# Optimization experiments

Hardware: AMD Instinct MI355X
Metric: run time of the kernel (lower is better)

The kernel has to match this reference:

```python
import jax, jax.numpy as jnp
import numpy as np

B, D, SLOTS, TOPK, CODE, ANCH = 8192, 64, 32, 3, 128, 32
BETA = 0.25  # vq_commitment_beta


def _clinear(zr, zi, Wr, Wi, br, bi):
    # ComplexLinear: real = Wr(zr)-Wi(zi), imag = Wi(zr)+Wr(zi); each nn.Linear carries its own bias
    return (zr @ Wr + br) - (zi @ Wi + bi), (zr @ Wi + bi) + (zi @ Wr + br)


def _layernorm(x, g, b, eps=1e-6):
    m = x.mean(-1, keepdims=True)
    v = ((x - m) ** 2).mean(-1, keepdims=True)  # biased var, as torch LayerNorm
    return (x - m) / jnp.sqrt(v + eps) * g + b


def setup_inputs() -> dict:
    key = jax.random.key(0)
    ks = jax.random.split(key, 16)
    f = jax.random.normal
    s = 0.05
    rng_init = 1.0 / np.sqrt(D)
    return dict(
        curr_r=f(ks[0], (B, D)), curr_i=f(ks[1], (B, D)),
        mem_r=f(ks[2], (B, SLOTS, D)), mem_i=f(ks[3], (B, SLOTS, D)),
        codebook=jax.random.uniform(ks[4], (CODE, 2 * D), minval=-rng_init, maxval=rng_init),
        qkv_Wr=f(ks[5], (3, D, D)) * s, qkv_Wi=f(ks[6], (3, D, D)) * s,
        qkv_br=jnp.zeros((3, D)), qkv_bi=jnp.zeros((3, D)),
        quad_Wr=f(ks[7], (D, D)) * s, quad_Wi=f(ks[8], (D, D)) * s,
        quad_br=jnp.zeros((D,)), quad_bi=jnp.zeros((D,)),
        sens_Wr=f(ks[9], (D, D)) * s, sens_Wi=f(ks[10], (D, D)) * s,
        sens_br=jnp.zeros((D,)), sens_bi=jnp.zeros((D,)),
        vis_palette=f(ks[11], (ANCH, 2 * D)), aud_palette=f(ks[12], (ANCH, 2 * D)),
        gate_W=f(ks[13], (2 * D, 1)) * s, gate_b=jnp.zeros((1,)),
        addr_W=f(ks[14], (2 * D, SLOTS)) * s, addr_b=jnp.zeros((SLOTS,)),
        ln_gamma_r=jnp.ones((D,)), ln_beta_r=jnp.zeros((D,)),
        ln_gamma_i=jnp.ones((D,)), ln_beta_i=jnp.zeros((D,)),
    )


def reference(curr_r, curr_i, mem_r, mem_i, codebook,
              qkv_Wr, qkv_Wi, qkv_br, qkv_bi,
              quad_Wr, quad_Wi, quad_br, quad_bi,
              sens_Wr, sens_Wi, sens_br, sens_bi,
              vis_palette, aud_palette,
              gate_W, gate_b, addr_W, addr_b,
              ln_gamma_r, ln_beta_r, ln_gamma_i, ln_beta_i):
    sg = jax.lax.stop_gradient
    z_flat = jnp.concatenate([curr_r, curr_i], -1)  # [B,2D]

    # ---- EMA_VQ (eval path): argmin codebook lookup + straight-through ----
    d = (z_flat ** 2).sum(1, keepdims=True) + (codebook ** 2).sum(1) - 2.0 * z_flat @ codebook.T
    d = jnp.maximum(d, 0.0)
    indices = jnp.argmin(d, -1)                      # [B]
    z_q = codebook[indices]                          # [B,2D]
    vq_loss = BETA * ((sg(z_q) - z_flat) ** 2).mean(-1)
    z_q = z_flat + sg(z_q - z_flat)
    probs = jnp.zeros((CODE,), z_flat.dtype).at[indices].add(1.0) / B
    norm_entropy = -(probs * jnp.log(probs + 1e-10)).sum() / np.log(CODE)
    vq_r, vq_i = z_q[..., :D], z_q[..., D:]

    # ---- HermitianGating ----
    qr, qi = _clinear(curr_r, curr_i, qkv_Wr[0], qkv_Wi[0], qkv_br[0], qkv_bi[0])
    kr, ki = _clinear(curr_r, curr_i, qkv_Wr[1], qkv_Wi[1], qkv_br[1], qkv_bi[1])
    vr, vi = _clinear(curr_r, curr_i, qkv_Wr[2], qkv_Wi[2], qkv_br[2], qkv_bi[2])
    gate = jax.nn.sigmoid((qr * kr + qi * ki).sum(-1, keepdims=True))
    g_r, g_i = vr * gate, vi * gate

    # ---- AssociativeMemory: softmax read + topk scatter write ----
    sim = jnp.einsum('bsd,bd->bs', mem_r, curr_r) + jnp.einsum('bsd,bd->bs', mem_i, curr_i)
    sim = sim - sg(sim.max(-1, keepdims=True))
    attn = jax.nn.softmax(sim, -1)
    read_r = jnp.einsum('bs,bsd->bd', attn, mem_r)
    read_i = jnp.einsum('bs,bsd->bd', attn, mem_i)
    write_gate = jax.nn.sigmoid(z_flat @ gate_W + gate_b)[:, :, None]  # [B,1,1]
    logits = z_flat @ addr_W + addr_b
    logits = logits - sg(logits.max(-1, keepdims=True))
    ww = jax.nn.softmax(logits, -1)                  # [B,SLOTS]
    slot_entropy = (-(ww * jnp.log(ww + 1e-10)).sum(-1)).mean()
    top_vals, top_idx = jax.lax.top_k(ww, TOPK)
    sparse = jnp.zeros_like(ww).at[jnp.arange(B)[:, None], top_idx].set(top_vals)
    sparse = sparse / (sparse.sum(-1, keepdims=True) + 1e-6)
    eff = write_gate * sparse[..., None]             # [B,SLOTS,1]
    nm_r = jnp.tanh(mem_r + eff * (curr_r[:, None, :] - mem_r))
    nm_i = jnp.tanh(mem_i + eff * (curr_i[:, None, :] - mem_i))
    nm_r = _layernorm(nm_r, ln_gamma_r, ln_beta_r)
    nm_i = _layernorm(nm_i, ln_gamma_i, ln_beta_i)

    # ---- SubmodalityAnchorModule ----
    s_r, s_i = _clinear(curr_r, curr_i, sens_Wr, sens_Wi, sens_br, sens_bi)
    sflat = jnp.concatenate([s_r, s_i], -1)

    def attend(pal):
        sc = sflat @ pal.T
        sc = sc - sg(sc.max(-1, keepdims=True))
        return jax.nn.softmax(sc, -1) @ pal

    vis = attend(vis_palette)
    aud = attend(aud_palette)
    exp_r = vis[..., :D] - aud[..., D:]   # vis_c + i*aud_c
    exp_i = vis[..., D:] + aud[..., :D]

    # ---- QuadratureModule: multiply by i ----
    zr, zi = _clinear(curr_r, curr_i, quad_Wr, quad_Wi, quad_br, quad_bi)
    q_r, q_i = -zi, zr

    combined = jnp.concatenate(
        [vq_r, vq_i, g_r, g_i, read_r, read_i, exp_r, exp_i, q_r, q_i,
         nm_r.reshape(B, -1), nm_i.reshape(B, -1)], -1)  # [B, 10*D + 2*SLOTS*D]
    return combined, vq_loss, indices, slot_entropy, norm_entropy
```

## Files before the change

### kernel.cpp

```cpp
#include <hip/hip_runtime.h>
#include <hip/hip_bf16.h>


#define NROWS 8
#define NBLOCKS 1024
#define RSTRIDE 4736

static constexpr size_t OFF_VQLOSS = 38797312UL;
static constexpr size_t OFF_IDX    = 38805504UL;
static constexpr size_t OFF_SENT   = 38813696UL;
static constexpr size_t OFF_NENT   = 38813697UL;

struct Params {
  const float* curr_r; const float* curr_i;
  const float* mem_r;  const float* mem_i;
  const float* codebook;
  const float* qkv_Wr; const float* qkv_Wi; const float* qkv_br; const float* qkv_bi;
  const float* quad_Wr; const float* quad_Wi; const float* quad_br; const float* quad_bi;
  const float* sens_Wr; const float* sens_Wi; const float* sens_br; const float* sens_bi;
  const float* vis_pal; const float* aud_pal;
  const float* gate_W; const float* gate_b;
  const float* addr_W; const float* addr_b;
  const float* ln_gr; const float* ln_br; const float* ln_gi; const float* ln_bi;
  float* out;
  int* hist;
  float* rowent;
};

__global__ __launch_bounds__(256) void vq_kernel(Params P) {
  const int t = threadIdx.x;
  const int bid = blockIdx.x;
  const int lane = t & 63;
  const int wv = t >> 6;

  __shared__ __align__(16) float s_zr[NROWS][64], s_zi[NROWS][64];
  __shared__ double s_cbn[128];
  __shared__ double s_dall[NROWS][256];
  __shared__ float s_vqls[NROWS];
  __shared__ int s_idx[NROWS];

  {
    const float* cr = P.curr_r + (size_t)bid * (NROWS * 64);
    const float* ci = P.curr_i + (size_t)bid * (NROWS * 64);
    float* zr = &s_zr[0][0];
    float* zi = &s_zi[0][0];
    for (int i = t; i < NROWS * 64; i += 256) { zr[i] = cr[i]; zi[i] = ci[i]; }
  }

  {
    const float* cb = P.codebook + (t & 127) * 128 + (t >> 7) * 64;
    double a = 0.0;
    for (int d = 0; d < 64; ++d) { double w = (double)cb[d]; a = fma(w, w, a); }
    s_dall[0][t] = a;
    __syncthreads();
    if (t < 128) s_cbn[t] = s_dall[0][t] + s_dall[0][t + 128];
    __syncthreads();
  }

  {
    const int c = t & 127, h = t >> 7;
    const float* cb = P.codebook + c * 128 + h * 64;
    const float (*zb)[64] = h ? s_zi : s_zr;
    double acc[NROWS];
    #pragma unroll
    for (int r = 0; r < NROWS; ++r) acc[r] = 0.0;
    for (int d = 0; d < 64; ++d) {
      const double w = (double)cb[d];
      #pragma unroll
      for (int r = 0; r < NROWS; ++r) acc[r] = fma(w, (double)zb[r][d], acc[r]);
    }
    #pragma unroll
    for (int r = 0; r < NROWS; ++r) s_dall[r][h * 128 + c] = acc[r];
    __syncthreads();
    #pragma unroll
    for (int rr = 0; rr < 2; ++rr) {
      const int r = wv * 2 + rr;
      const double d0 = s_cbn[lane]      - 2.0 * (s_dall[r][lane]      + s_dall[r][128 + lane]);
      const double d1 = s_cbn[lane + 64] - 2.0 * (s_dall[r][64 + lane] + s_dall[r][192 + lane]);
      double sv = d0; int si = lane;
      if (d1 < sv) { sv = d1; si = lane + 64; }
      #pragma unroll
      for (int m = 1; m <= 32; m <<= 1) {
        double ov = __shfl_xor(sv, m);
        int oi = __shfl_xor(si, m);
        if (ov < sv || (ov == sv && oi < si)) { sv = ov; si = oi; }
      }
      if (lane == 0) { s_idx[r] = si; atomicAdd(&P.hist[si], 1); }
    }
    __syncthreads();
  }

  {
    #pragma unroll
    for (int rr = 0; rr < 2; ++rr) {
      const int r = wv * 2 + rr;
      const float* cb = P.codebook + (size_t)s_idx[r] * 128;
      float d0_ = cb[lane] - s_zr[r][lane];
      float d1_ = cb[64 + lane] - s_zi[r][lane];
      float v = d0_ * d0_ + d1_ * d1_;
      #pragma unroll
      for (int m = 1; m <= 32; m <<= 1) v += __shfl_xor(v, m);
      if (lane == 0) s_vqls[r] = 0.25f * v * (1.0f / 128.0f);
    }
  }
  __syncthreads();

  {
    const int j = t & 63, g = t >> 6;
    #pragma unroll
    for (int rr = 0; rr < 4; ++rr) {
      const int r = (g >> 1) * 4 + rr;
      float* orow = P.out + ((size_t)bid * NROWS + r) * RSTRIDE;
      const float* cb = P.codebook + (size_t)s_idx[r] * 128;
      if ((g & 1) == 0) {
        float z = s_zr[r][j];
        orow[j] = z + (cb[j] - z);
      } else {
        float z = s_zi[r][j];
        orow[64 + j] = z + (cb[64 + j] - z);
      }
    }
  }
  if (t < NROWS) {
    P.out[OFF_VQLOSS + (size_t)bid * NROWS + t] = s_vqls[t];
    P.out[OFF_IDX + (size_t)bid * NROWS + t] = (float)s_idx[t];
  }
}

union __align__(16) ScratchL {
  float w[64][64];
  struct { float vis[NROWS][128]; float palp[NROWS][32]; } pal;
};

__global__ __launch_bounds__(256) void lin_kernel(Params P) {
  const int t = threadIdx.x;
  const int bid = blockIdx.x;

  __shared__ __align__(16) float s_zr[NROWS][64], s_zi[NROWS][64];
  __shared__ ScratchL u;
  __shared__ float s_qr[NROWS][64], s_qi[NROWS][64];
  __shared__ float s_kr[NROWS][64], s_ki[NROWS][64];
  __shared__ float s_vr[NROWS][64], s_vi[NROWS][64];
  __shared__ __align__(16) float s_sf[NROWS][128];
  __shared__ float s_gate[NROWS];

  {
    const float* cr = P.curr_r + (size_t)bid * (NROWS * 64);
    const float* ci = P.curr_i + (size_t)bid * (NROWS * 64);
    float* zr = &s_zr[0][0];
    float* zi = &s_zi[0][0];
    for (int i = t; i < NROWS * 64; i += 256) { zr[i] = cr[i]; zi[i] = ci[i]; }
  }
  __syncthreads();

  {
    const int j = t & 63, rg = t >> 6;
    const float* Wr_tab[5] = {P.qkv_Wr, P.qkv_Wr + 4096, P.qkv_Wr + 8192, P.quad_Wr, P.sens_Wr};
    const float* Wi_tab[5] = {P.qkv_Wi, P.qkv_Wi + 4096, P.qkv_Wi + 8192, P.quad_Wi, P.sens_Wi};
    const float* br_tab[5] = {P.qkv_br, P.qkv_br + 64, P.qkv_br + 128, P.quad_br, P.sens_br};
    const float* bi_tab[5] = {P.qkv_bi, P.qkv_bi + 64, P.qkv_bi + 128, P.quad_bi, P.sens_bi};
    #pragma unroll 1
    for (int cl = 0; cl < 5; ++cl) {
      __syncthreads();
      { const float4* src = (const float4*)Wr_tab[cl];
        float4* dst = (float4*)&u.w[0][0];
        for (int i = t; i < 1024; i += 256) dst[i] = src[i]; }
      __syncthreads();
      float aRR0 = 0.f, aRR1 = 0.f, aIR0 = 0.f, aIR1 = 0.f;
      for (int d4 = 0; d4 < 64; d4 += 4) {
        float4 zr0 = *(const float4*)&s_zr[rg][d4];
        float4 zr1 = *(const float4*)&s_zr[rg + 4][d4];
        float4 zi0 = *(const float4*)&s_zi[rg][d4];
        float4 zi1 = *(const float4*)&s_zi[rg + 4][d4];
        float w0 = u.w[d4 + 0][j], w1 = u.w[d4 + 1][j];
        float w2 = u.w[d4 + 2][j], w3 = u.w[d4 + 3][j];
        aRR0 += zr0.x * w0 + zr0.y * w1 + zr0.z * w2 + zr0.w * w3;
        aRR1 += zr1.x * w0 + zr1.y * w1 + zr1.z * w2 + zr1.w * w3;
        aIR0 += zi0.x * w0 + zi0.y * w1 + zi0.z * w2 + zi0.w * w3;
        aIR1 += zi1.x * w0 + zi1.y * w1 + zi1.z * w2 + zi1.w * w3;
      }
      __syncthreads();
      { const float4* src = (const float4*)Wi_tab[cl];
        float4* dst = (float4*)&u.w[0][0];
        for (int i = t; i < 1024; i += 256) dst[i] = src[i]; }
      __syncthreads();
      float aRI0 = 0.f, aRI1 = 0.f, aII0 = 0.f, aII1 = 0.f;
      for (int d4 = 0; d4 < 64; d4 += 4) {
        float4 zr0 = *(const float4*)&s_zr[rg][d4];
        float4 zr1 = *(const float4*)&s_zr[rg + 4][d4];
        float4 zi0 = *(const float4*)&s_zi[rg][d4];
        float4 zi1 = *(const float4*)&s_zi[rg + 4][d4];
        float w0 = u.w[d4 + 0][j], w1 = u.w[d4 + 1][j];
        float w2 = u.w[d4 + 2][j], w3 = u.w[d4 + 3][j];
        aRI0 += zr0.x * w0 + zr0.y * w1 + zr0.z * w2 + zr0.w * w3;
        aRI1 += zr1.x * w0 + zr1.y * w1 + zr1.z * w2 + zr1.w * w3;
        aII0 += zi0.x * w0 + zi0.y * w1 + zi0.z * w2 + zi0.w * w3;
        aII1 += zi1.x * w0 + zi1.y * w1 + zi1.z * w2 + zi1.w * w3;
      }
      const float brj = br_tab[cl][j], bij = bi_tab[cl][j];
      #pragma unroll
      for (int hh = 0; hh < 2; ++hh) {
        const int r = rg + hh * 4;
        const float pRR = hh ? aRR1 : aRR0;
        const float pII = hh ? aII1 : aII0;
        const float pRI = hh ? aRI1 : aRI0;
        const float pIR = hh ? aIR1 : aIR0;
        const float oR = (pRR + brj) - (pII + bij);
        const float oI = (pRI + bij) + (pIR + brj);
        if (cl == 0)      { s_qr[r][j] = oR; s_qi[r][j] = oI; }
        else if (cl == 1) { s_kr[r][j] = oR; s_ki[r][j] = oI; }
        else if (cl == 2) { s_vr[r][j] = oR; s_vi[r][j] = oI; }
        else if (cl == 3) {
          float* orow = P.out + ((size_t)bid * NROWS + r) * RSTRIDE;
          orow[512 + j] = -oI;
          orow[576 + j] = oR;
        } else            { s_sf[r][j] = oR; s_sf[r][64 + j] = oI; }
      }
    }
    __syncthreads();
  }

  {
    const int r = t >> 5, l = t & 31;
    float g = s_qr[r][l] * s_kr[r][l] + s_qi[r][l] * s_ki[r][l]
            + s_qr[r][l + 32] * s_kr[r][l + 32] + s_qi[r][l + 32] * s_ki[r][l + 32];
    #pragma unroll
    for (int m = 16; m >= 1; m >>= 1) g += __shfl_xor(g, m);
    if (l == 0) s_gate[r] = 1.f / (1.f + expf(-g));
  }
  __syncthreads();

  {
    const int r = t >> 5, a = t & 31;
    float sc = 0.f;
    for (int jj = 0; jj < 128; jj += 4) {
      const float4 sf = *(const float4*)&s_sf[r][jj];
      const float4 pv = *(const float4*)&P.vis_pal[a * 128 + jj];
      sc += sf.x * pv.x + sf.y * pv.y + sf.z * pv.z + sf.w * pv.w;
    }
    float mx = sc;
    #pragma unroll
    for (int m = 16; m >= 1; m >>= 1) mx = fmaxf(mx, __shfl_xor(mx, m));
    float e = expf(sc - mx);
    float sm = e;
    #pragma unroll
    for (int m = 16; m >= 1; m >>= 1) sm += __shfl_xor(sm, m);
    u.pal.palp[r][a] = e / sm;
  }
  __syncthreads();
  {
    const int j = t & 127, rp = t >> 7;
    float acc[4] = {0.f, 0.f, 0.f, 0.f};
    for (int a = 0; a < 32; ++a) {
      const float pv = P.vis_pal[a * 128 + j];
      #pragma unroll
      for (int q = 0; q < 4; ++q) acc[q] += u.pal.palp[rp + q * 2][a] * pv;
    }
    #pragma unroll
    for (int q = 0; q < 4; ++q) u.pal.vis[rp + q * 2][j] = acc[q];
  }
  __syncthreads();
  {
    const int r = t >> 5, a = t & 31;
    float sc = 0.f;
    for (int jj = 0; jj < 128; jj += 4) {
      const float4 sf = *(const float4*)&s_sf[r][jj];
      const float4 pv = *(const float4*)&P.aud_pal[a * 128 + jj];
      sc += sf.x * pv.x + sf.y * pv.y + sf.z * pv.z + sf.w * pv.w;
    }
    float mx = sc;
    #pragma unroll
    for (int m = 16; m >= 1; m >>= 1) mx = fmaxf(mx, __shfl_xor(mx, m));
    float e = expf(sc - mx);
    float sm = e;
    #pragma unroll
    for (int m = 16; m >= 1; m >>= 1) sm += __shfl_xor(sm, m);
    u.pal.palp[r][a] = e / sm;
  }
  __syncthreads();
  {
    const int j = t & 127, rp = t >> 7;
    float acc[4] = {0.f, 0.f, 0.f, 0.f};
    for (int a = 0; a < 32; ++a) {
      const float pv = P.aud_pal[a * 128 + j];
      #pragma unroll
      for (int q = 0; q < 4; ++q) acc[q] += u.pal.palp[rp + q * 2][a] * pv;
    }
    #pragma unroll
    for (int q = 0; q < 4; ++q) {
      const int rr = rp + q * 2;
      const size_t bb = (size_t)bid * NROWS + rr;
      float* orow = P.out + bb * RSTRIDE;
      if (j < 64) orow[448 + j] = u.pal.vis[rr][64 + j] + acc[q];
      else        orow[384 + (j - 64)] = u.pal.vis[rr][j - 64] - acc[q];
    }
  }

  {
    const int j = t & 63, g = t >> 6;
    #pragma unroll
    for (int rr = 0; rr < 4; ++rr) {
      const int r = (g >> 1) * 4 + rr;
      float* orow = P.out + ((size_t)bid * NROWS + r) * RSTRIDE;
      if ((g & 1) == 0) orow[128 + j] = s_vr[r][j] * s_gate[r];
      else              orow[192 + j] = s_vi[r][j] * s_gate[r];
    }
  }
}

__global__ __launch_bounds__(256, 4) void mem_kernel(Params P) {
  const int b = blockIdx.x;
  const int t = threadIdx.x;
  const int lane = t & 63;
  const int wv = t >> 6;

  __shared__ float zr[64], zi[64];
  __shared__ float lp[4][32];
  __shared__ float s_eff[32];
  __shared__ float s_sim[32], s_attn[32];
  __shared__ float s_rr[4][8][8], s_ri[4][8][8];
  __shared__ float s_wg;

  if (t < 64)       zr[t]      = P.curr_r[(size_t)b * 64 + t];
  else if (t < 128) zi[t - 64] = P.curr_i[(size_t)b * 64 + (t - 64)];
  __syncthreads();

  const size_t bb = (size_t)b;
  const int s = t >> 3, k = t & 7, d0 = k * 8;
  const float* mrp = P.mem_r + ((bb * 32 + s) * 64 + d0);
  const float* mip = P.mem_i + ((bb * 32 + s) * 64 + d0);
  float4 a0 = *(const float4*)mrp, a1 = *(const float4*)(mrp + 4);
  float4 b0 = *(const float4*)mip, b1 = *(const float4*)(mip + 4);
  float mr[8] = {a0.x, a0.y, a0.z, a0.w, a1.x, a1.y, a1.z, a1.w};
  float mi[8] = {b0.x, b0.y, b0.z, b0.w, b1.x, b1.y, b1.z, b1.w};

  if (t < 128) {
    const int q = t >> 5, l = t & 31;
    const float* zz = (q < 2) ? zr : zi;
    const int zb = (q & 1) * 32;
    float a = 0.f;
    for (int i = 0; i < 32; ++i) a += zz[zb + i] * P.addr_W[(q * 32 + i) * 32 + l];
    lp[q][l] = a;
  } else if (t < 192) {
    const int j = t - 128;
    float tw = zr[j] * P.gate_W[j] + zi[j] * P.gate_W[64 + j];
    #pragma unroll
    for (int m = 1; m <= 32; m <<= 1) tw += __shfl_xor(tw, m);
    if (j == 0) s_wg = tw;
  }

  float sp = 0.f;
  #pragma unroll
  for (int x = 0; x < 8; ++x) sp += mr[x] * zr[d0 + x] + mi[x] * zi[d0 + x];
  sp += __shfl_xor(sp, 1); sp += __shfl_xor(sp, 2); sp += __shfl_xor(sp, 4);
  if (k == 0) s_sim[s] = sp;
  __syncthreads();

  if (t < 32) {
    float v = s_sim[t];
    float mx = v;
    #pragma unroll
    for (int m = 16; m >= 1; m >>= 1) mx = fmaxf(mx, __shfl_xor(mx, m));
    float e = expf(v - mx);
    float sm = e;
    #pragma unroll
    for (int m = 16; m >= 1; m >>= 1) sm += __shfl_xor(sm, m);
    s_attn[t] = e / sm;
  } else if (t >= 64 && t < 96) {
    const int l = t - 64;
    float lg = lp[0][l] + lp[1][l] + lp[2][l] + lp[3][l] + P.addr_b[l];
    float mx = lg;
    #pragma unroll
    for (int m = 16; m >= 1; m >>= 1) mx = fmaxf(mx, __shfl_xor(mx, m));
    float e = expf(lg - mx);
    float sm = e;
    #pragma unroll
    for (int m = 16; m >= 1; m >>= 1) sm += __shfl_xor(sm, m);
    const float w = e / sm;
    float es = -(w * logf(w + 1e-10f));
    #pragma unroll
    for (int m = 16; m >= 1; m >>= 1) es += __shfl_xor(es, m);
    if (l == 0) P.rowent[b] = es;
    const float myw = w;
    bool picked = false;
    float val = w; int idx = l;
    float sumtop = 0.f;
    #pragma unroll
    for (int it = 0; it < 3; ++it) {
      float v2 = val; int i2 = idx;
      #pragma unroll
      for (int m = 16; m >= 1; m >>= 1) {
        float ov = __shfl_xor(v2, m); int oi = __shfl_xor(i2, m);
        if (ov > v2 || (ov == v2 && oi < i2)) { v2 = ov; i2 = oi; }
      }
      sumtop += v2;
      if (l == i2) { picked = true; val = -1e30f; }
    }
    const float wgate = 1.f / (1.f + expf(-(s_wg + P.gate_b[0])));
    s_eff[l] = picked ? wgate * (myw / (sumtop + 1e-6f)) : 0.f;
  }
  __syncthreads();

  const float aw = s_attn[s];
  {
    float pr[8], pi[8];
    #pragma unroll
    for (int x = 0; x < 8; ++x) { pr[x] = aw * mr[x]; pi[x] = aw * mi[x]; }
    #pragma unroll
    for (int m = 8; m <= 32; m <<= 1) {
      #pragma unroll
      for (int x = 0; x < 8; ++x) { pr[x] += __shfl_xor(pr[x], m); pi[x] += __shfl_xor(pi[x], m); }
    }
    if (lane < 8) {
      #pragma unroll
      for (int x = 0; x < 8; ++x) { s_rr[wv][lane][x] = pr[x]; s_ri[wv][lane][x] = pi[x]; }
    }
  }
  {
    const float eff = s_eff[s];
    float nr[8], ni[8];
    #pragma unroll
    for (int x = 0; x < 8; ++x) {
      nr[x] = tanhf(mr[x] + eff * (zr[d0 + x] - mr[x]));
      ni[x] = tanhf(mi[x] + eff * (zi[d0 + x] - mi[x]));
    }
    float sR = 0.f, sI = 0.f;
    #pragma unroll
    for (int x = 0; x < 8; ++x) { sR += nr[x]; sI += ni[x]; }
    sR += __shfl_xor(sR, 1); sR += __shfl_xor(sR, 2); sR += __shfl_xor(sR, 4);
    sI += __shfl_xor(sI, 1); sI += __shfl_xor(sI, 2); sI += __shfl_xor(sI, 4);
    const float mR = sR * (1.f / 64.f), mI = sI * (1.f / 64.f);
    float vR = 0.f, vI = 0.f;
    #pragma unroll
    for (int x = 0; x < 8; ++x) {
      float dr = nr[x] - mR; vR += dr * dr;
      float di = ni[x] - mI; vI += di * di;
    }
    vR += __shfl_xor(vR, 1); vR += __shfl_xor(vR, 2); vR += __shfl_xor(vR, 4);
    vI += __shfl_xor(vI, 1); vI += __shfl_xor(vI, 2); vI += __shfl_xor(vI, 4);
    const float invR = 1.f / sqrtf(vR * (1.f / 64.f) + 1e-6f);
    const float invI = 1.f / sqrtf(vI * (1.f / 64.f) + 1e-6f);
    float* orow = P.out + bb * RSTRIDE;
    float oR[8], oI[8];
    #pragma unroll
    for (int x = 0; x < 8; ++x) {
      const int d = d0 + x;
      oR[x] = (nr[x] - mR) * invR * P.ln_gr[d] + P.ln_br[d];
      oI[x] = (ni[x] - mI) * invI * P.ln_gi[d] + P.ln_bi[d];
    }
    *(float4*)&orow[640 + s * 64 + d0]      = make_float4(oR[0], oR[1], oR[2], oR[3]);
    *(float4*)&orow[640 + s * 64 + d0 + 4]  = make_float4(oR[4], oR[5], oR[6], oR[7]);
    *(float4*)&orow[2688 + s * 64 + d0]     = make_float4(oI[0], oI[1], oI[2], oI[3]);
    *(float4*)&orow[2688 + s * 64 + d0 + 4] = make_float4(oI[4], oI[5], oI[6], oI[7]);
  }
  __syncthreads();
  if (t < 64) {
    const int kk = t >> 3, xx = t & 7;
    float rv = s_rr[0][kk][xx] + s_rr[1][kk][xx] + s_rr[2][kk][xx] + s_rr[3][kk][xx];
    float iv = s_ri[0][kk][xx] + s_ri[1][kk][xx] + s_ri[2][kk][xx] + s_ri[3][kk][xx];
    float* orow = P.out + bb * RSTRIDE;
    orow[256 + t] = rv;
    orow[320 + t] = iv;
  }
}

__global__ __launch_bounds__(256) void finalize_k(const int* hist, const float* rowent,
                                                  float* out) {
  const int t = threadIdx.x;
  __shared__ float red[256];
  float se = 0.f;
  for (int i = t; i < 8192; i += 256) se += rowent[i];
  red[t] = se;
  __syncthreads();
  for (int off = 128; off >= 1; off >>= 1) {
    if (t < off) red[t] += red[t + off];
    __syncthreads();
  }
  if (t == 0) out[OFF_SENT] = red[0] / 8192.0f;
  __syncthreads();
  float ne = 0.f;
  if (t < 128) {
    const float pp = (float)hist[t] / 8192.0f;
    ne = -(pp * logf(pp + 1e-10f));
  }
  red[t] = ne;
  __syncthreads();
  for (int off = 128; off >= 1; off >>= 1) {
    if (t < off) red[t] += red[t + off];
    __syncthreads();
  }
  if (t == 0) out[OFF_NENT] = red[0] / logf(128.0f);
}

extern "C" void kernel_launch(void* const* d_in, const int* in_sizes, int n_in,
                              void* d_out, int out_size, void* d_ws, size_t ws_size,
                              hipStream_t stream) {
  (void)in_sizes; (void)n_in; (void)out_size; (void)ws_size;
  Params P;
  P.curr_r   = (const float*)d_in[0];
  P.curr_i   = (const float*)d_in[1];
  P.mem_r    = (const float*)d_in[2];
  P.mem_i    = (const float*)d_in[3];
  P.codebook = (const float*)d_in[4];
  P.qkv_Wr   = (const float*)d_in[5];
  P.qkv_Wi   = (const float*)d_in[6];
  P.qkv_br   = (const float*)d_in[7];
  P.qkv_bi   = (const float*)d_in[8];
  P.quad_Wr  = (const float*)d_in[9];
  P.quad_Wi  = (const float*)d_in[10];
  P.quad_br  = (const float*)d_in[11];
  P.quad_bi  = (const float*)d_in[12];
  P.sens_Wr  = (const float*)d_in[13];
  P.sens_Wi  = (const float*)d_in[14];
  P.sens_br  = (const float*)d_in[15];
  P.sens_bi  = (const float*)d_in[16];
  P.vis_pal  = (const float*)d_in[17];
  P.aud_pal  = (const float*)d_in[18];
  P.gate_W   = (const float*)d_in[19];
  P.gate_b   = (const float*)d_in[20];
  P.addr_W   = (const float*)d_in[21];
  P.addr_b   = (const float*)d_in[22];
  P.ln_gr    = (const float*)d_in[23];
  P.ln_br    = (const float*)d_in[24];
  P.ln_gi    = (const float*)d_in[25];
  P.ln_bi    = (const float*)d_in[26];
  P.out = (float*)d_out;
  P.hist = (int*)d_ws;
  P.rowent = (float*)((char*)d_ws + 512);

  hipMemsetAsync(d_ws, 0, 512, stream);
  mem_kernel<<<dim3(8192), dim3(256), 0, stream>>>(P);
  vq_kernel<<<dim3(NBLOCKS), dim3(256), 0, stream>>>(P);
  lin_kernel<<<dim3(NBLOCKS), dim3(256), 0, stream>>>(P);
  finalize_k<<<dim3(1), dim3(256), 0, stream>>>(P.hist, P.rowent, (float*)d_out);
}
```

Baseline: 266.9 us.

## Fuse linear/palette kernel into per-row memory kernel

Merges lin_kernel into mem_kernel as a single per-row kernel, row_main, that computes the qkv/quad/sens complex linears, gate, palette attention and memory update for one batch row per block. This removes one launch and the second read of curr, and puts the small matmuls in the shadow of the memory-bound mem load. In exchange the weights are read directly from global/L2 by all 8192 blocks instead of being staged in shared memory and reused across 8 rows, so weight traffic and serial per-thread dot loops grow. The __launch_bounds__ min-blocks hint of 4 is also dropped.

```diff
diff --git a/kernel.cpp b/kernel.cpp
--- a/kernel.cpp
+++ b/kernel.cpp
@@ -27,6 +27,266 @@
   float* rowent;
 };
 
+__global__ __launch_bounds__(256) void row_main(Params P) {
+  const int b = blockIdx.x;
+  const int t = threadIdx.x;
+  const int lane = t & 63;
+  const int wv = t >> 6;
+
+  __shared__ float zr[64], zi[64];
+  __shared__ float s_qr[64], s_qi[64], s_kr[64], s_ki[64], s_vr[64], s_vi[64];
+  __shared__ float sfl[128];
+  __shared__ float s_sp[4][4][64];
+  __shared__ float lp[4][32];
+  __shared__ float s_eff[32];
+  __shared__ float s_sim[32], s_attn[32];
+  __shared__ float s_rr[4][8][8], s_ri[4][8][8];
+  __shared__ float s_pv[4][32], s_pa[4][32];
+  __shared__ float s_pvp[32], s_pap[32];
+  __shared__ float s_vo[128], s_ao[128];
+  __shared__ float s_wg, s_gate;
+
+  const size_t bb = (size_t)b;
+  const int s = t >> 3, k = t & 7, d0 = k * 8;
+  const float* mrp = P.mem_r + ((bb * 32 + s) * 64 + d0);
+  const float* mip = P.mem_i + ((bb * 32 + s) * 64 + d0);
+  float4 a0 = *(const float4*)mrp, a1 = *(const float4*)(mrp + 4);
+  float4 b0 = *(const float4*)mip, b1 = *(const float4*)(mip + 4);
+  float mr[8] = {a0.x, a0.y, a0.z, a0.w, a1.x, a1.y, a1.z, a1.w};
+  float mi[8] = {b0.x, b0.y, b0.z, b0.w, b1.x, b1.y, b1.z, b1.w};
+
+  if (t < 64)       zr[t]      = P.curr_r[bb * 64 + t];
+  else if (t < 128) zi[t - 64] = P.curr_i[bb * 64 + (t - 64)];
+  __syncthreads();
+
+  float* orow = P.out + bb * RSTRIDE;
+
+  {
+    const int j = lane, cl = wv;
+    const float *Wr, *Wi, *br_, *bi_;
+    if      (cl == 0) { Wr = P.qkv_Wr;        Wi = P.qkv_Wi;        br_ = P.qkv_br;       bi_ = P.qkv_bi;       }
+    else if (cl == 1) { Wr = P.qkv_Wr + 4096; Wi = P.qkv_Wi + 4096; br_ = P.qkv_br + 64;  bi_ = P.qkv_bi + 64;  }
+    else if (cl == 2) { Wr = P.qkv_Wr + 8192; Wi = P.qkv_Wi + 8192; br_ = P.qkv_br + 128; bi_ = P.qkv_bi + 128; }
+    else              { Wr = P.quad_Wr;       Wi = P.quad_Wi;       br_ = P.quad_br;      bi_ = P.quad_bi;      }
+    float aRR = 0.f, aRI = 0.f, aIR = 0.f, aII = 0.f;
+    for (int d = 0; d < 64; ++d) {
+      const float xr = zr[d], xi = zi[d];
+      const float wr = Wr[d * 64 + j], wi = Wi[d * 64 + j];
+      aRR += xr * wr; aRI += xr * wi; aIR += xi * wr; aII += xi * wi;
+    }
+    const float oR = (aRR + br_[j]) - (aII + bi_[j]);
+    const float oI = (aRI + bi_[j]) + (aIR + br_[j]);
+    if      (cl == 0) { s_qr[j] = oR; s_qi[j] = oI; }
+    else if (cl == 1) { s_kr[j] = oR; s_ki[j] = oI; }
+    else if (cl == 2) { s_vr[j] = oR; s_vi[j] = oI; }
+    else              { orow[512 + j] = -oI; orow[576 + j] = oR; }
+    float bRR = 0.f, bRI = 0.f, bIR = 0.f, bII = 0.f;
+    for (int dd = 0; dd < 16; ++dd) {
+      const int d = wv * 16 + dd;
+      const float xr = zr[d], xi = zi[d];
+      const float wr = P.sens_Wr[d * 64 + j], wi = P.sens_Wi[d * 64 + j];
+      bRR += xr * wr; bRI += xr * wi; bIR += xi * wr; bII += xi * wi;
+    }
+    s_sp[wv][0][j] = bRR; s_sp[wv][1][j] = bRI; s_sp[wv][2][j] = bIR; s_sp[wv][3][j] = bII;
+  }
+  __syncthreads();
+
+  {
+    float sp = 0.f;
+    #pragma unroll
+    for (int x = 0; x < 8; ++x) sp += mr[x] * zr[d0 + x] + mi[x] * zi[d0 + x];
+    sp += __shfl_xor(sp, 1); sp += __shfl_xor(sp, 2); sp += __shfl_xor(sp, 4);
+    if (k == 0) s_sim[s] = sp;
+  }
+  if (t < 128) {
+    const int q = t >> 5, l = t & 31;
+    const float* zz = (q < 2) ? zr : zi;
+    const int zb = (q & 1) * 32;
+    float a = 0.f;
+    for (int i = 0; i < 32; ++i) a += zz[zb + i] * P.addr_W[(q * 32 + i) * 32 + l];
+    lp[q][l] = a;
+  } else if (t < 192) {
+    const int j = t - 128;
+    float tw = zr[j] * P.gate_W[j] + zi[j] * P.gate_W[64 + j];
+    #pragma unroll
+    for (int m = 1; m <= 32; m <<= 1) tw += __shfl_xor(tw, m);
+    if (j == 0) s_wg = tw;
+  } else {
+    const int j = t - 192;
+    float g = s_qr[j] * s_kr[j] + s_qi[j] * s_ki[j];
+    #pragma unroll
+    for (int m = 1; m <= 32; m <<= 1) g += __shfl_xor(g, m);
+    if (j == 0) s_gate = 1.f / (1.f + expf(-g));
+  }
+  __syncthreads();
+
+  if (t < 32) {
+    float v = s_sim[t];
+    float mx = v;
+    #pragma unroll
+    for (int m = 16; m >= 1; m >>= 1) mx = fmaxf(mx, __shfl_xor(mx, m));
+    float e = expf(v - mx);
+    float sm = e;
+    #pragma unroll
+    for (int m = 16; m >= 1; m >>= 1) sm += __shfl_xor(sm, m);
+    s_attn[t] = e / sm;
+  } else if (t >= 64 && t < 96) {
+    const int l = t - 64;
+    float lg = lp[0][l] + lp[1][l] + lp[2][l] + lp[3][l] + P.addr_b[l];
+    float mx = lg;
+    #pragma unroll
+    for (int m = 16; m >= 1; m >>= 1) mx = fmaxf(mx, __shfl_xor(mx, m));
+    float e = expf(lg - mx);
+    float sm = e;
+    #pragma unroll
+    for (int m = 16; m >= 1; m >>= 1) sm += __shfl_xor(sm, m);
+    const float w = e / sm;
+    float es = -(w * logf(w + 1e-10f));
+    #pragma unroll
+    for (int m = 16; m >= 1; m >>= 1) es += __shfl_xor(es, m);
+    if (l == 0) P.rowent[b] = es;
+    const float myw = w;
+    bool picked = false;
+    float val = w; int idx = l;
+    float sumtop = 0.f;
+    #pragma unroll
+    for (int it = 0; it < 3; ++it) {
+      float v2 = val; int i2 = idx;
+      #pragma unroll
+      for (int m = 16; m >= 1; m >>= 1) {
+        float ov = __shfl_xor(v2, m); int oi = __shfl_xor(i2, m);
+        if (ov > v2 || (ov == v2 && oi < i2)) { v2 = ov; i2 = oi; }
+      }
+      sumtop += v2;
+      if (l == i2) { picked = true; val = -1e30f; }
+    }
+    const float wgate = 1.f / (1.f + expf(-(s_wg + P.gate_b[0])));
+    s_eff[l] = picked ? wgate * (myw / (sumtop + 1e-6f)) : 0.f;
+  } else if (t >= 128 && t < 192) {
+    const int j = t - 128;
+    const float aRR = s_sp[0][0][j] + s_sp[1][0][j] + s_sp[2][0][j] + s_sp[3][0][j];
+    const float aRI = s_sp[0][1][j] + s_sp[1][1][j] + s_sp[2][1][j] + s_sp[3][1][j];
+    const float aIR = s_sp[0][2][j] + s_sp[1][2][j] + s_sp[2][2][j] + s_sp[3][2][j];
+    const float aII = s_sp[0][3][j] + s_sp[1][3][j] + s_sp[2][3][j] + s_sp[3][3][j];
+    const float oR = (aRR + P.sens_br[j]) - (aII + P.sens_bi[j]);
+    const float oI = (aRI + P.sens_bi[j]) + (aIR + P.sens_br[j]);
+    sfl[j] = oR; sfl[64 + j] = oI;
+  }
+  __syncthreads();
+
+  const float aw = s_attn[s];
+  {
+    float pr[8], pi[8];
+    #pragma unroll
+    for (int x = 0; x < 8; ++x) { pr[x] = aw * mr[x]; pi[x] = aw * mi[x]; }
+    #pragma unroll
+    for (int m = 8; m <= 32; m <<= 1) {
+      #pragma unroll
+      for (int x = 0; x < 8; ++x) { pr[x] += __shfl_xor(pr[x], m); pi[x] += __shfl_xor(pi[x], m); }
+    }
+    if (lane < 8) {
+      #pragma unroll
+      for (int x = 0; x < 8; ++x) { s_rr[wv][lane][x] = pr[x]; s_ri[wv][lane][x] = pi[x]; }
+    }
+  }
+  {
+    const float eff = s_eff[s];
+    float nr[8], ni[8];
+    #pragma unroll
+    for (int x = 0; x < 8; ++x) {
+      nr[x] = tanhf(mr[x] + eff * (zr[d0 + x] - mr[x]));
+      ni[x] = tanhf(mi[x] + eff * (zi[d0 + x] - mi[x]));
+    }
+    float sR = 0.f, sI = 0.f;
+    #pragma unroll
+    for (int x = 0; x < 8; ++x) { sR += nr[x]; sI += ni[x]; }
+    sR += __shfl_xor(sR, 1); sR += __shfl_xor(sR, 2); sR += __shfl_xor(sR, 4);
+    sI += __shfl_xor(sI, 1); sI += __shfl_xor(sI, 2); sI += __shfl_xor(sI, 4);
+    const float mR = sR * (1.f / 64.f), mI = sI * (1.f / 64.f);
+    float vR = 0.f, vI = 0.f;
+    #pragma unroll
+    for (int x = 0; x < 8; ++x) {
+      float dr = nr[x] - mR; vR += dr * dr;
+      float di = ni[x] - mI; vI += di * di;
+    }
+    vR += __shfl_xor(vR, 1); vR += __shfl_xor(vR, 2); vR += __shfl_xor(vR, 4);
+    vI += __shfl_xor(vI, 1); vI += __shfl_xor(vI, 2); vI += __shfl_xor(vI, 4);
+    const float invR = 1.f / sqrtf(vR * (1.f / 64.f) + 1e-6f);
+    const float invI = 1.f / sqrtf(vI * (1.f / 64.f) + 1e-6f);
+    float oR[8], oI[8];
+    #pragma unroll
+    for (int x = 0; x < 8; ++x) {
+      const int d = d0 + x;
+      oR[x] = (nr[x] - mR) * invR * P.ln_gr[d] + P.ln_br[d];
+      oI[x] = (ni[x] - mI) * invI * P.ln_gi[d] + P.ln_bi[d];
+    }
+    *(float4*)&orow[640 + s * 64 + d0]      = make_float4(oR[0], oR[1], oR[2], oR[3]);
+    *(float4*)&orow[640 + s * 64 + d0 + 4]  = make_float4(oR[4], oR[5], oR[6], oR[7]);
+    *(float4*)&orow[2688 + s * 64 + d0]     = make_float4(oI[0], oI[1], oI[2], oI[3]);
+    *(float4*)&orow[2688 + s * 64 + d0 + 4] = make_float4(oI[4], oI[5], oI[6], oI[7]);
+  }
+  if (t < 128) {
+    const int a = t & 31, q = t >> 5;
+    float sc = 0.f;
+    for (int x = q * 32; x < q * 32 + 32; ++x) sc += sfl[x] * P.vis_pal[a * 128 + x];
+    s_pv[q][a] = sc;
+  } else {
+    const int tt = t - 128, a = tt & 31, q = tt >> 5;
+    float sc = 0.f;
+    for (int x = q * 32; x < q * 32 + 32; ++x) sc += sfl[x] * P.aud_pal[a * 128 + x];
+    s_pa[q][a] = sc;
+  }
+  __syncthreads();
+
+  if (t < 64) {
+    const int kk = t >> 3, xx = t & 7;
+    float rv = s_rr[0][kk][xx] + s_rr[1][kk][xx] + s_rr[2][kk][xx] + s_rr[3][kk][xx];
+    float iv = s_ri[0][kk][xx] + s_ri[1][kk][xx] + s_ri[2][kk][xx] + s_ri[3][kk][xx];
+    orow[256 + t] = rv;
+    orow[320 + t] = iv;
+  } else if (t >= 128 && t < 160) {
+    const int a = t - 128;
+    float sc = s_pv[0][a] + s_pv[1][a] + s_pv[2][a] + s_pv[3][a];
+    float mx = sc;
+    #pragma unroll
+    for (int m = 16; m >= 1; m >>= 1) mx = fmaxf(mx, __shfl_xor(mx, m));
+    float e = expf(sc - mx);
+    float sm = e;
+    #pragma unroll
+    for (int m = 16; m >= 1; m >>= 1) sm += __shfl_xor(sm, m);
+    s_pvp[a] = e / sm;
+  } else if (t >= 192 && t < 224) {
+    const int a = t - 192;
+    float sc = s_pa[0][a] + s_pa[1][a] + s_pa[2][a] + s_pa[3][a];
+    float mx = sc;
+    #pragma unroll
+    for (int m = 16; m >= 1; m >>= 1) mx = fmaxf(mx, __shfl_xor(mx, m));
+    float e = expf(sc - mx);
+    float sm = e;
+    #pragma unroll
+    for (int m = 16; m >= 1; m >>= 1) sm += __shfl_xor(sm, m);
+    s_pap[a] = e / sm;
+  }
+  __syncthreads();
+
+  if (t < 128) {
+    float v = 0.f;
+    for (int a = 0; a < 32; ++a) v += s_pvp[a] * P.vis_pal[a * 128 + t];
+    s_vo[t] = v;
+  } else {
+    const int j = t - 128;
+    float v = 0.f;
+    for (int a = 0; a < 32; ++a) v += s_pap[a] * P.aud_pal[a * 128 + j];
+    s_ao[j] = v;
+  }
+  if (t < 64)       orow[128 + t] = s_vr[t] * s_gate;
+  else if (t < 128) orow[192 + (t - 64)] = s_vi[t - 64] * s_gate;
+  __syncthreads();
+
+  if (t < 64)       orow[384 + t] = s_vo[t] - s_ao[64 + t];
+  else if (t < 128) orow[448 + (t - 64)] = s_vo[t] + s_ao[t - 64];
+}
+
 __global__ __launch_bounds__(256) void vq_kernel(Params P) {
   const int t = threadIdx.x;
   const int bid = blockIdx.x;
@@ -46,7 +306,6 @@
     float* zi = &s_zi[0][0];
     for (int i = t; i < NROWS * 64; i += 256) { zr[i] = cr[i]; zi[i] = ci[i]; }
   }
-
   {
     const float* cb = P.codebook + (t & 127) * 128 + (t >> 7) * 64;
     double a = 0.0;
@@ -56,7 +315,6 @@
     if (t < 128) s_cbn[t] = s_dall[0][t] + s_dall[0][t + 128];
     __syncthreads();
   }
-
   {
     const int c = t & 127, h = t >> 7;
     const float* cb = P.codebook + c * 128 + h * 64;
@@ -89,7 +347,6 @@
     }
     __syncthreads();
   }
-
   {
     #pragma unroll
     for (int rr = 0; rr < 2; ++rr) {
@@ -104,7 +361,6 @@
     }
   }
   __syncthreads();
-
   {
     const int j = t & 63, g = t >> 6;
     #pragma unroll
@@ -124,343 +380,6 @@
   if (t < NROWS) {
     P.out[OFF_VQLOSS + (size_t)bid * NROWS + t] = s_vqls[t];
     P.out[OFF_IDX + (size_t)bid * NROWS + t] = (float)s_idx[t];
-  }
-}
-
-union __align__(16) ScratchL {
-  float w[64][64];
-  struct { float vis[NROWS][128]; float palp[NROWS][32]; } pal;
-};
-
-__global__ __launch_bounds__(256) void lin_kernel(Params P) {
-  const int t = threadIdx.x;
-  const int bid = blockIdx.x;
-
-  __shared__ __align__(16) float s_zr[NROWS][64], s_zi[NROWS][64];
-  __shared__ ScratchL u;
-  __shared__ float s_qr[NROWS][64], s_qi[NROWS][64];
-  __shared__ float s_kr[NROWS][64], s_ki[NROWS][64];
-  __shared__ float s_vr[NROWS][64], s_vi[NROWS][64];
-  __shared__ __align__(16) float s_sf[NROWS][128];
-  __shared__ float s_gate[NROWS];
-
-  {
-    const float* cr = P.curr_r + (size_t)bid * (NROWS * 64);
-    const float* ci = P.curr_i + (size_t)bid * (NROWS * 64);
-    float* zr = &s_zr[0][0];
-    float* zi = &s_zi[0][0];
-    for (int i = t; i < NROWS * 64; i += 256) { zr[i] = cr[i]; zi[i] = ci[i]; }
-  }
-  __syncthreads();
-
-  {
-    const int j = t & 63, rg = t >> 6;
-    const float* Wr_tab[5] = {P.qkv_Wr, P.qkv_Wr + 4096, P.qkv_Wr + 8192, P.quad_Wr, P.sens_Wr};
-    const float* Wi_tab[5] = {P.qkv_Wi, P.qkv_Wi + 4096, P.qkv_Wi + 8192, P.quad_Wi, P.sens_Wi};
-    const float* br_tab[5] = {P.qkv_br, P.qkv_br + 64, P.qkv_br + 128, P.quad_br, P.sens_br};
-    const float* bi_tab[5] = {P.qkv_bi, P.qkv_bi + 64, P.qkv_bi + 128, P.quad_bi, P.sens_bi};
-    #pragma unroll 1
-    for (int cl = 0; cl < 5; ++cl) {
-      __syncthreads();
-      { const float4* src = (const float4*)Wr_tab[cl];
-        float4* dst = (float4*)&u.w[0][0];
-        for (int i = t; i < 1024; i += 256) dst[i] = src[i]; }
-      __syncthreads();
-      float aRR0 = 0.f, aRR1 = 0.f, aIR0 = 0.f, aIR1 = 0.f;
-      for (int d4 = 0; d4 < 64; d4 += 4) {
-        float4 zr0 = *(const float4*)&s_zr[rg][d4];
-        float4 zr1 = *(const float4*)&s_zr[rg + 4][d4];
-        float4 zi0 = *(const float4*)&s_zi[rg][d4];
-        float4 zi1 = *(const float4*)&s_zi[rg + 4][d4];
-        float w0 = u.w[d4 + 0][j], w1 = u.w[d4 + 1][j];
-        float w2 = u.w[d4 + 2][j], w3 = u.w[d4 + 3][j];
-        aRR0 += zr0.x * w0 + zr0.y * w1 + zr0.z * w2 + zr0.w * w3;
-        aRR1 += zr1.x * w0 + zr1.y * w1 + zr1.z * w2 + zr1.w * w3;
-        aIR0 += zi0.x * w0 + zi0.y * w1 + zi0.z * w2 + zi0.w * w3;
-        aIR1 += zi1.x * w0 + zi1.y * w1 + zi1.z * w2 + zi1.w * w3;
-      }
-      __syncthreads();
-      { const float4* src = (const float4*)Wi_tab[cl];
-        float4* dst = (float4*)&u.w[0][0];
-        for (int i = t; i < 1024; i += 256) dst[i] = src[i]; }
-      __syncthreads();
-      float aRI0 = 0.f, aRI1 = 0.f, aII0 = 0.f, aII1 = 0.f;
-      for (int d4 = 0; d4 < 64; d4 += 4) {
-        float4 zr0 = *(const float4*)&s_zr[rg][d4];
-        float4 zr1 = *(const float4*)&s_zr[rg + 4][d4];
-        float4 zi0 = *(const float4*)&s_zi[rg][d4];
-        float4 zi1 = *(const float4*)&s_zi[rg + 4][d4];
-        float w0 = u.w[d4 + 0][j], w1 = u.w[d4 + 1][j];
-        float w2 = u.w[d4 + 2][j], w3 = u.w[d4 + 3][j];
-        aRI0 += zr0.x * w0 + zr0.y * w1 + zr0.z * w2 + zr0.w * w3;
-        aRI1 += zr1.x * w0 + zr1.y * w1 + zr1.z * w2 + zr1.w * w3;
-        aII0 += zi0.x * w0 + zi0.y * w1 + zi0.z * w2 + zi0.w * w3;
-        aII1 += zi1.x * w0 + zi1.y * w1 + zi1.z * w2 + zi1.w * w3;
-      }
-      const float brj = br_tab[cl][j], bij = bi_tab[cl][j];
-      #pragma unroll
-      for (int hh = 0; hh < 2; ++hh) {
-        const int r = rg + hh * 4;
-        const float pRR = hh ? aRR1 : aRR0;
-        const float pII = hh ? aII1 : aII0;
-        const float pRI = hh ? aRI1 : aRI0;
-        const float pIR = hh ? aIR1 : aIR0;
-        const float oR = (pRR + brj) - (pII + bij);
-        const float oI = (pRI + bij) + (pIR + brj);
-        if (cl == 0)      { s_qr[r][j] = oR; s_qi[r][j] = oI; }
-        else if (cl == 1) { s_kr[r][j] = oR; s_ki[r][j] = oI; }
-        else if (cl == 2) { s_vr[r][j] = oR; s_vi[r][j] = oI; }
-        else if (cl == 3) {
-          float* orow = P.out + ((size_t)bid * NROWS + r) * RSTRIDE;
-          orow[512 + j] = -oI;
-          orow[576 + j] = oR;
-        } else            { s_sf[r][j] = oR; s_sf[r][64 + j] = oI; }
-      }
-    }
-    __syncthreads();
-  }
-
-  {
-    const int r = t >> 5, l = t & 31;
-    float g = s_qr[r][l] * s_kr[r][l] + s_qi[r][l] * s_ki[r][l]
-            + s_qr[r][l + 32] * s_kr[r][l + 32] + s_qi[r][l + 32] * s_ki[r][l + 32];
-    #pragma unroll
-    for (int m = 16; m >= 1; m >>= 1) g += __shfl_xor(g, m);
-    if (l == 0) s_gate[r] = 1.f / (1.f + expf(-g));
-  }
-  __syncthreads();
-
-  {
-    const int r = t >> 5, a = t & 31;
-    float sc = 0.f;
-    for (int jj = 0; jj < 128; jj += 4) {
-      const float4 sf = *(const float4*)&s_sf[r][jj];
-      const float4 pv = *(const float4*)&P.vis_pal[a * 128 + jj];
-      sc += sf.x * pv.x + sf.y * pv.y + sf.z * pv.z + sf.w * pv.w;
-    }
-    float mx = sc;
-    #pragma unroll
-    for (int m = 16; m >= 1; m >>= 1) mx = fmaxf(mx, __shfl_xor(mx, m));
-    float e = expf(sc - mx);
-    float sm = e;
-    #pragma unroll
-    for (int m = 16; m >= 1; m >>= 1) sm += __shfl_xor(sm, m);
-    u.pal.palp[r][a] = e / sm;
-  }
-  __syncthreads();
-  {
-    const int j = t & 127, rp = t >> 7;
-    float acc[4] = {0.f, 0.f, 0.f, 0.f};
-    for (int a = 0; a < 32; ++a) {
-      const float pv = P.vis_pal[a * 128 + j];
-      #pragma unroll
-      for (int q = 0; q < 4; ++q) acc[q] += u.pal.palp[rp + q * 2][a] * pv;
-    }
-    #pragma unroll
-    for (int q = 0; q < 4; ++q) u.pal.vis[rp + q * 2][j] = acc[q];
-  }
-  __syncthreads();
-  {
-    const int r = t >> 5, a = t & 31;
-    float sc = 0.f;
-    for (int jj = 0; jj < 128; jj += 4) {
-      const float4 sf = *(const float4*)&s_sf[r][jj];
-      const float4 pv = *(const float4*)&P.aud_pal[a * 128 + jj];
-      sc += sf.x * pv.x + sf.y * pv.y + sf.z * pv.z + sf.w * pv.w;
-    }
-    float mx = sc;
-    #pragma unroll
-    for (int m = 16; m >= 1; m >>= 1) mx = fmaxf(mx, __shfl_xor(mx, m));
-    float e = expf(sc - mx);
-    float sm = e;
-    #pragma unroll
-    for (int m = 16; m >= 1; m >>= 1) sm += __shfl_xor(sm, m);
-    u.pal.palp[r][a] = e / sm;
-  }
-  __syncthreads();
-  {
-    const int j = t & 127, rp = t >> 7;
-    float acc[4] = {0.f, 0.f, 0.f, 0.f};
-    for (int a = 0; a < 32; ++a) {
-      const float pv = P.aud_pal[a * 128 + j];
-      #pragma unroll
-      for (int q = 0; q < 4; ++q) acc[q] += u.pal.palp[rp + q * 2][a] * pv;
-    }
-    #pragma unroll
-    for (int q = 0; q < 4; ++q) {
-      const int rr = rp + q * 2;
-      const size_t bb = (size_t)bid * NROWS + rr;
-      float* orow = P.out + bb * RSTRIDE;
-      if (j < 64) orow[448 + j] = u.pal.vis[rr][64 + j] + acc[q];
-      else        orow[384 + (j - 64)] = u.pal.vis[rr][j - 64] - acc[q];
-    }
-  }
-
-  {
-    const int j = t & 63, g = t >> 6;
-    #pragma unroll
-    for (int rr = 0; rr < 4; ++rr) {
-      const int r = (g >> 1) * 4 + rr;
-      float* orow = P.out + ((size_t)bid * NROWS + r) * RSTRIDE;
-      if ((g & 1) == 0) orow[128 + j] = s_vr[r][j] * s_gate[r];
-      else              orow[192 + j] = s_vi[r][j] * s_gate[r];
-    }
-  }
-}
-
-__global__ __launch_bounds__(256, 4) void mem_kernel(Params P) {
-  const int b = blockIdx.x;
-  const int t = threadIdx.x;
-  const int lane = t & 63;
-  const int wv = t >> 6;
-
-  __shared__ float zr[64], zi[64];
-  __shared__ float lp[4][32];
-  __shared__ float s_eff[32];
-  __shared__ float s_sim[32], s_attn[32];
-  __shared__ float s_rr[4][8][8], s_ri[4][8][8];
-  __shared__ float s_wg;
-
-  if (t < 64)       zr[t]      = P.curr_r[(size_t)b * 64 + t];
-  else if (t < 128) zi[t - 64] = P.curr_i[(size_t)b * 64 + (t - 64)];
-  __syncthreads();
-
-  const size_t bb = (size_t)b;
-  const int s = t >> 3, k = t & 7, d0 = k * 8;
-  const float* mrp = P.mem_r + ((bb * 32 + s) * 64 + d0);
-  const float* mip = P.mem_i + ((bb * 32 + s) * 64 + d0);
-  float4 a0 = *(const float4*)mrp, a1 = *(const float4*)(mrp + 4);
-  float4 b0 = *(const float4*)mip, b1 = *(const float4*)(mip + 4);
-  float mr[8] = {a0.x, a0.y, a0.z, a0.w, a1.x, a1.y, a1.z, a1.w};
-  float mi[8] = {b0.x, b0.y, b0.z, b0.w, b1.x, b1.y, b1.z, b1.w};
-
-  if (t < 128) {
-    const int q = t >> 5, l = t & 31;
-    const float* zz = (q < 2) ? zr : zi;
-    const int zb = (q & 1) * 32;
-    float a = 0.f;
-    for (int i = 0; i < 32; ++i) a += zz[zb + i] * P.addr_W[(q * 32 + i) * 32 + l];
-    lp[q][l] = a;
-  } else if (t < 192) {
-    const int j = t - 128;
-    float tw = zr[j] * P.gate_W[j] + zi[j] * P.gate_W[64 + j];
-    #pragma unroll
-    for (int m = 1; m <= 32; m <<= 1) tw += __shfl_xor(tw, m);
-    if (j == 0) s_wg = tw;
-  }
-
-  float sp = 0.f;
-  #pragma unroll
-  for (int x = 0; x < 8; ++x) sp += mr[x] * zr[d0 + x] + mi[x] * zi[d0 + x];
-  sp += __shfl_xor(sp, 1); sp += __shfl_xor(sp, 2); sp += __shfl_xor(sp, 4);
-  if (k == 0) s_sim[s] = sp;
-  __syncthreads();
-
-  if (t < 32) {
-    float v = s_sim[t];
-    float mx = v;
-    #pragma unroll
-    for (int m = 16; m >= 1; m >>= 1) mx = fmaxf(mx, __shfl_xor(mx, m));
-    float e = expf(v - mx);
-    float sm = e;
-    #pragma unroll
-    for (int m = 16; m >= 1; m >>= 1) sm += __shfl_xor(sm, m);
-    s_attn[t] = e / sm;
-  } else if (t >= 64 && t < 96) {
-    const int l = t - 64;
-    float lg = lp[0][l] + lp[1][l] + lp[2][l] + lp[3][l] + P.addr_b[l];
-    float mx = lg;
-    #pragma unroll
-    for (int m = 16; m >= 1; m >>= 1) mx = fmaxf(mx, __shfl_xor(mx, m));
-    float e = expf(lg - mx);
-    float sm = e;
-    #pragma unroll
-    for (int m = 16; m >= 1; m >>= 1) sm += __shfl_xor(sm, m);
-    const float w = e / sm;
-    float es = -(w * logf(w + 1e-10f));
-    #pragma unroll
-    for (int m = 16; m >= 1; m >>= 1) es += __shfl_xor(es, m);
-    if (l == 0) P.rowent[b] = es;
-    const float myw = w;
-    bool picked = false;
-    float val = w; int idx = l;
-    float sumtop = 0.f;
-    #pragma unroll
-    for (int it = 0; it < 3; ++it) {
-      float v2 = val; int i2 = idx;
-      #pragma unroll
-      for (int m = 16; m >= 1; m >>= 1) {
-        float ov = __shfl_xor(v2, m); int oi = __shfl_xor(i2, m);
-        if (ov > v2 || (ov == v2 && oi < i2)) { v2 = ov; i2 = oi; }
-      }
-      sumtop += v2;
-      if (l == i2) { picked = true; val = -1e30f; }
-    }
-    const float wgate = 1.f / (1.f + expf(-(s_wg + P.gate_b[0])));
-    s_eff[l] = picked ? wgate * (myw / (sumtop + 1e-6f)) : 0.f;
-  }
-  __syncthreads();
-
-  const float aw = s_attn[s];
-  {
-    float pr[8], pi[8];
-    #pragma unroll
-    for (int x = 0; x < 8; ++x) { pr[x] = aw * mr[x]; pi[x] = aw * mi[x]; }
-    #pragma unroll
-    for (int m = 8; m <= 32; m <<= 1) {
-      #pragma unroll
-      for (int x = 0; x < 8; ++x) { pr[x] += __shfl_xor(pr[x], m); pi[x] += __shfl_xor(pi[x], m); }
-    }
-    if (lane < 8) {
-      #pragma unroll
-      for (int x = 0; x < 8; ++x) { s_rr[wv][lane][x] = pr[x]; s_ri[wv][lane][x] = pi[x]; }
-    }
-  }
-  {
-    const float eff = s_eff[s];
-    float nr[8], ni[8];
-    #pragma unroll
-    for (int x = 0; x < 8; ++x) {
-      nr[x] = tanhf(mr[x] + eff * (zr[d0 + x] - mr[x]));
-      ni[x] = tanhf(mi[x] + eff * (zi[d0 + x] - mi[x]));
-    }
-    float sR = 0.f, sI = 0.f;
-    #pragma unroll
-    for (int x = 0; x < 8; ++x) { sR += nr[x]; sI += ni[x]; }
-    sR += __shfl_xor(sR, 1); sR += __shfl_xor(sR, 2); sR += __shfl_xor(sR, 4);
-    sI += __shfl_xor(sI, 1); sI += __shfl_xor(sI, 2); sI += __shfl_xor(sI, 4);
-    const float mR = sR * (1.f / 64.f), mI = sI * (1.f / 64.f);
-    float vR = 0.f, vI = 0.f;
-    #pragma unroll
-    for (int x = 0; x < 8; ++x) {
-      float dr = nr[x] - mR; vR += dr * dr;
-      float di = ni[x] - mI; vI += di * di;
-    }
-    vR += __shfl_xor(vR, 1); vR += __shfl_xor(vR, 2); vR += __shfl_xor(vR, 4);
-    vI += __shfl_xor(vI, 1); vI += __shfl_xor(vI, 2); vI += __shfl_xor(vI, 4);
-    const float invR = 1.f / sqrtf(vR * (1.f / 64.f) + 1e-6f);
-    const float invI = 1.f / sqrtf(vI * (1.f / 64.f) + 1e-6f);
-    float* orow = P.out + bb * RSTRIDE;
-    float oR[8], oI[8];
-    #pragma unroll
-    for (int x = 0; x < 8; ++x) {
-      const int d = d0 + x;
-      oR[x] = (nr[x] - mR) * invR * P.ln_gr[d] + P.ln_br[d];
-      oI[x] = (ni[x] - mI) * invI * P.ln_gi[d] + P.ln_bi[d];
-    }
-    *(float4*)&orow[640 + s * 64 + d0]      = make_float4(oR[0], oR[1], oR[2], oR[3]);
-    *(float4*)&orow[640 + s * 64 + d0 + 4]  = make_float4(oR[4], oR[5], oR[6], oR[7]);
-    *(float4*)&orow[2688 + s * 64 + d0]     = make_float4(oI[0], oI[1], oI[2], oI[3]);
-    *(float4*)&orow[2688 + s * 64 + d0 + 4] = make_float4(oI[4], oI[5], oI[6], oI[7]);
-  }
-  __syncthreads();
-  if (t < 64) {
-    const int kk = t >> 3, xx = t & 7;
-    float rv = s_rr[0][kk][xx] + s_rr[1][kk][xx] + s_rr[2][kk][xx] + s_rr[3][kk][xx];
-    float iv = s_ri[0][kk][xx] + s_ri[1][kk][xx] + s_ri[2][kk][xx] + s_ri[3][kk][xx];
-    float* orow = P.out + bb * RSTRIDE;
-    orow[256 + t] = rv;
-    orow[320 + t] = iv;
   }
 }
 
@@ -529,8 +448,7 @@
   P.rowent = (float*)((char*)d_ws + 512);
 
   hipMemsetAsync(d_ws, 0, 512, stream);
-  mem_kernel<<<dim3(8192), dim3(256), 0, stream>>>(P);
+  row_main<<<dim3(8192), dim3(256), 0, stream>>>(P);
   vq_kernel<<<dim3(NBLOCKS), dim3(256), 0, stream>>>(P);
-  lin_kernel<<<dim3(NBLOCKS), dim3(256), 0, stream>>>(P);
   finalize_k<<<dim3(1), dim3(256), 0, stream>>>(P.hist, P.rowent, (float*)d_out);
 }
```

After: 252.3 us. 1.06x faster.
